# Kernel tuning notes

Hardware: AMD Instinct MI355X
Metric: run time of the kernel (lower is better)

Reference implementation:

```python
import jax, jax.numpy as jnp
import numpy as np

B, S, C = 16, 1024, 1024
E, H = 1024, 16
DH = E // H

def setup_inputs() -> dict:
    key = jax.random.key(0)
    k1, k2, k3, k4, k5 = jax.random.split(key, 5)
    x = jax.random.normal(k1, (B, S, C), dtype=jnp.float32)
    # learned params, sized per init_kwargs (torch Linear default init scale ~ 1/sqrt(fan_in))
    w_qkv = jax.random.normal(k2, (C, 3 * E), dtype=jnp.float32) / np.sqrt(C)
    b_qkv = jax.random.normal(k3, (3 * E,), dtype=jnp.float32) * 0.01
    w_o = jax.random.normal(k4, (E, E), dtype=jnp.float32) / np.sqrt(E)
    b_o = jax.random.normal(k5, (E,), dtype=jnp.float32) * 0.01
    return {"x": x, "w_qkv": w_qkv, "b_qkv": b_qkv, "w_o": w_o, "b_o": b_o}

def reference(x, w_qkv, b_qkv, w_o, b_o):
    b, s, _ = x.shape
    # fused QKV projection: [B,S,3E] -> [B,S,H,3*Dh]
    qkv = (jnp.einsum('bsc,ce->bse', x, w_qkv) + b_qkv).reshape(b, s, H, 3 * DH)
    q, k, v = jnp.split(qkv, 3, axis=-1)  # each [B,S,H,Dh]
    # NOTE: faithful to source — attention over the HEADS axis at each position,
    # scaled by embed_size**-0.5 (not head_dim).
    attn = jnp.einsum('bshd,bstd->bsht', q, k) * (E ** -0.5)  # [B,S,H,H]
    attn = jax.nn.softmax(attn, axis=-1)
    out = jnp.einsum('bsht,bstd->bshd', attn, v).reshape(b, s, E)
    return jnp.einsum('bse,ef->bsf', out, w_o) + b_o
```

## Files before the change

kernel.cpp:

```cpp
#include <hip/hip_runtime.h>
#include <hip/hip_bf16.h>
#include <stdint.h>

#define DEVINLINE __device__ __forceinline__

typedef __attribute__((ext_vector_type(4))) float f32x4;
typedef __attribute__((ext_vector_type(8))) short bf16x8;

DEVINLINE unsigned short f2bf(float f) {
    union { float f; uint32_t u; } v; v.f = f;
    uint32_t u = v.u;
    uint32_t rounding = 0x7FFFu + ((u >> 16) & 1u);
    u += rounding;
    return (unsigned short)(u >> 16);
}

DEVINLINE float bf2f(unsigned short h) {
    union { uint32_t u; float f; } v; v.u = ((uint32_t)h) << 16;
    return v.f;
}

__global__ void cvt_f32_bf16(const float* __restrict__ in,
                             unsigned short* __restrict__ out, int n) {
    int i = (blockIdx.x * blockDim.x + threadIdx.x) * 4;
    int stride = gridDim.x * blockDim.x * 4;
    for (; i < n; i += stride) {
        float4 v = *reinterpret_cast<const float4*>(in + i);
        ushort4 o;
        o.x = f2bf(v.x); o.y = f2bf(v.y); o.z = f2bf(v.z); o.w = f2bf(v.w);
        *reinterpret_cast<ushort4*>(out + i) = o;
    }
}

__global__ void transpose_cvt(const float* __restrict__ in,
                              unsigned short* __restrict__ out,
                              int R, int Ccols) {
    __shared__ float tile[32][33];
    int c0 = blockIdx.x * 32, r0 = blockIdx.y * 32;
    int tx = threadIdx.x, ty = threadIdx.y;
    #pragma unroll
    for (int j = 0; j < 32; j += 8)
        tile[ty + j][tx] = in[(size_t)(r0 + ty + j) * Ccols + c0 + tx];
    __syncthreads();
    #pragma unroll
    for (int j = 0; j < 32; j += 8)
        out[(size_t)(c0 + ty + j) * R + r0 + tx] = f2bf(tile[tx][ty + j]);
}


#define GLD(srcp, dstp) __builtin_amdgcn_global_load_lds( \
    (const __attribute__((address_space(1))) void*)(srcp), \
    (__attribute__((address_space(3))) void*)(dstp), 16, 0, 0)

#define STAGE(P, regionUS, srcBase, row0, kkE) do { \
    const unsigned short* _s = (srcBase) + (size_t)(row0) * K + (kkE); \
    unsigned short* _d = lds + (P) * 32768 + (regionUS) + wid * 512; \
    GLD(_s, _d); GLD(_s + (size_t)64 * K, _d + 4096); } while (0)

#define RD_A(dst, AS0, AS1, h) do { _Pragma("unroll") \
    for (int _i = 0; _i < 4; ++_i) { \
        dst[_i][0] = *(const bf16x8*)((AS0) + ((h) * 8192 + _i * 2048)); \
        dst[_i][1] = *(const bf16x8*)((AS1) + ((h) * 8192 + _i * 2048)); } } while (0)

#define RD_B(dst, BS0, BS1, nh) do { _Pragma("unroll") \
    for (int _j = 0; _j < 2; ++_j) { \
        dst[_j][0] = *(const bf16x8*)((BS0) + ((nh) * 4096 + _j * 2048)); \
        dst[_j][1] = *(const bf16x8*)((BS1) + ((nh) * 4096 + _j * 2048)); } } while (0)

#define MMA(aX, bY, mh, nh) do { \
    __builtin_amdgcn_s_setprio(1); \
    _Pragma("unroll") for (int _i = 0; _i < 4; ++_i) { \
    _Pragma("unroll") for (int _j = 0; _j < 2; ++_j) { \
        acc[(mh)*4+_i][(nh)*2+_j] = __builtin_amdgcn_mfma_f32_16x16x32_bf16( \
            aX[_i][0], bY[_j][0], acc[(mh)*4+_i][(nh)*2+_j], 0, 0, 0); \
        acc[(mh)*4+_i][(nh)*2+_j] = __builtin_amdgcn_mfma_f32_16x16x32_bf16( \
            aX[_i][1], bY[_j][1], acc[(mh)*4+_i][(nh)*2+_j], 0, 0, 0); } } \
    __builtin_amdgcn_s_setprio(0); } while (0)

#define VM4 asm volatile("s_waitcnt vmcnt(4)" ::: "memory")
#define BAR() asm volatile("s_barrier" ::: "memory")

#define KTILE(AS0c, AS1c, BS0c, BS1c, AS0n, AS1n, BS0n, BS1n, Pc, kk) do { \
    MMA(aA, bA, 0, 0); \
    RD_B(bB, BS0c, BS1c, 1); \
    BAR(); \
    MMA(aA, bB, 0, 1); \
    RD_A(aB, AS0c, AS1c, 1); \
    VM4; BAR(); \
    MMA(aB, bA, 1, 0); \
    RD_B(bA, BS0n, BS1n, 0); \
    STAGE(Pc, 16384, bSrc, 0,   kk); \
    STAGE(Pc, 24576, bSrc, 128, kk); \
    VM4; BAR(); \
    MMA(aB, bB, 1, 1); \
    RD_A(aA, AS0n, AS1n, 0); \
    STAGE(Pc, 0,     aSrc, 0,   kk); \
    STAGE(Pc, 8192,  aSrc, 128, kk); \
    BAR(); } while (0)

template <bool OUT_BF16>
__launch_bounds__(512, 2)
__global__ void gemm256(const unsigned short* __restrict__ A,
                        const unsigned short* __restrict__ Bt,
                        const float* __restrict__ bias,
                        void* __restrict__ Cout,
                        int M, int N, int K, int NTN) {
    __shared__ unsigned short lds[65536];
    const int NT = K >> 6;

    int t = threadIdx.x;
    int wid = t >> 6, lane = t & 63;
    int wr = wid >> 2, wc = wid & 3;
    int fr = lane & 15, fq = lane >> 4;

    int nwg = gridDim.x, bid = blockIdx.x;
    int cpx = nwg >> 3;
    int swz = (bid & 7) * cpx + (bid >> 3);
    int tm = swz / NTN, tn = swz % NTN;
    int bm = tm * 256, bn = tn * 256;

    int rowl = t >> 3, col8 = t & 7;
    int swzcol = (col8 ^ (rowl & 7)) << 3;
    const unsigned short* aSrc = A + (size_t)(bm + rowl) * K + swzcol;
    const unsigned short* bSrc = Bt + (size_t)(bn + rowl) * K + swzcol;

    int swzm = (fr & 7) << 3;
    int colS0 = (fq << 3) ^ swzm;
    int colS1 = (32 | (fq << 3)) ^ swzm;

    char* ldsb = (char*)lds;
    char* A00 = ldsb + ((wr * 128 + fr) << 7) + 2 * colS0;
    char* A10 = ldsb + ((wr * 128 + fr) << 7) + 2 * colS1;
    char* B00 = ldsb + ((256 + wc * 64 + fr) << 7) + 2 * colS0;
    char* B10 = ldsb + ((256 + wc * 64 + fr) << 7) + 2 * colS1;
    char* A01 = A00 + 65536; char* A11 = A10 + 65536;
    char* B01 = B00 + 65536; char* B11 = B10 + 65536;

    f32x4 acc[8][4] = {};
    bf16x8 aA[4][2], aB[4][2], bA[2][2], bB[2][2];

    STAGE(0, 0,     aSrc, 0,   0);
    STAGE(0, 8192,  aSrc, 128, 0);
    STAGE(0, 16384, bSrc, 0,   0);
    STAGE(0, 24576, bSrc, 128, 0);
    STAGE(1, 16384, bSrc, 0,   64);
    STAGE(1, 24576, bSrc, 128, 64);
    STAGE(1, 0,     aSrc, 0,   64);
    STAGE(1, 8192,  aSrc, 128, 64);
    asm volatile("s_waitcnt vmcnt(8)" ::: "memory");
    BAR();
    RD_A(aA, A00, A10, 0);
    RD_B(bA, B00, B10, 0);

    for (int tau = 0; tau < NT; tau += 2) {
        int kkA = ((tau + 2 < NT) ? (tau + 2) : (NT - 1)) << 6;
        KTILE(A00, A10, B00, B10, A01, A11, B01, B11, 0, kkA);
        int kkB = ((tau + 3 < NT) ? (tau + 3) : (NT - 1)) << 6;
        KTILE(A01, A11, B01, B11, A00, A10, B00, B10, 1, kkB);
    }
    asm volatile("s_waitcnt vmcnt(0)" ::: "memory");

    #pragma unroll
    for (int m = 0; m < 8; ++m) {
        #pragma unroll
        for (int n = 0; n < 4; ++n) {
            int col = bn + wc * 64 + n * 16 + fr;
            float bv = bias[col];
            #pragma unroll
            for (int r = 0; r < 4; ++r) {
                int row = bm + wr * 128 + m * 16 + fq * 4 + r;
                float v = acc[m][n][r] + bv;
                if (OUT_BF16)
                    ((unsigned short*)Cout)[(size_t)row * N + col] = f2bf(v);
                else
                    ((float*)Cout)[(size_t)row * N + col] = v;
            }
        }
    }
}

__global__ __launch_bounds__(256)
void attn_kernel(const unsigned short* __restrict__ qkv,
                 unsigned short* __restrict__ out) {
    __shared__ float sv[4][16][68];
    __shared__ float sp[4][16][17];
    int wv = threadIdx.x >> 6;
    int l = threadIdx.x & 63;
    int pos = blockIdx.x * 4 + wv;
    const unsigned short* rowp = qkv + (size_t)pos * 3072;

    #pragma unroll
    for (int j = 0; j < 2; ++j) {
        int i8 = (j * 64 + l) * 8;
        int h = i8 >> 6, d = i8 & 63;
        ushort4 v0 = *reinterpret_cast<const ushort4*>(rowp + h * 192 + 128 + d);
        ushort4 v1 = *reinterpret_cast<const ushort4*>(rowp + h * 192 + 128 + d + 4);
        sv[wv][h][d + 0] = bf2f(v0.x); sv[wv][h][d + 1] = bf2f(v0.y);
        sv[wv][h][d + 2] = bf2f(v0.z); sv[wv][h][d + 3] = bf2f(v0.w);
        sv[wv][h][d + 4] = bf2f(v1.x); sv[wv][h][d + 5] = bf2f(v1.y);
        sv[wv][h][d + 6] = bf2f(v1.z); sv[wv][h][d + 7] = bf2f(v1.w);
    }

    int fr = l & 15, fq = l >> 4;
    const unsigned short* hb = rowp + fr * 192 + fq * 8;
    bf16x8 kf0 = *reinterpret_cast<const bf16x8*>(hb + 64);
    bf16x8 kf1 = *reinterpret_cast<const bf16x8*>(hb + 96);
    bf16x8 qf0 = *reinterpret_cast<const bf16x8*>(hb);
    bf16x8 qf1 = *reinterpret_cast<const bf16x8*>(hb + 32);
    f32x4 st = {};
    st = __builtin_amdgcn_mfma_f32_16x16x32_bf16(kf0, qf0, st, 0, 0, 0);
    st = __builtin_amdgcn_mfma_f32_16x16x32_bf16(kf1, qf1, st, 0, 0, 0);

    float s0 = st[0] * 0.03125f, s1 = st[1] * 0.03125f;
    float s2 = st[2] * 0.03125f, s3 = st[3] * 0.03125f;
    float m = fmaxf(fmaxf(s0, s1), fmaxf(s2, s3));
    m = fmaxf(m, __shfl_xor(m, 16));
    m = fmaxf(m, __shfl_xor(m, 32));
    float e0 = __expf(s0 - m), e1 = __expf(s1 - m);
    float e2 = __expf(s2 - m), e3 = __expf(s3 - m);
    float sum = e0 + e1 + e2 + e3;
    sum += __shfl_xor(sum, 16);
    sum += __shfl_xor(sum, 32);
    float inv = 1.0f / sum;
    sp[wv][fr][fq * 4 + 0] = e0 * inv;
    sp[wv][fr][fq * 4 + 1] = e1 * inv;
    sp[wv][fr][fq * 4 + 2] = e2 * inv;
    sp[wv][fr][fq * 4 + 3] = e3 * inv;
    __syncthreads();

    int h2 = l >> 2, tq = l & 3;
    int dbase = tq * 16;
    float4 o0 = {}, o1 = {}, o2 = {}, o3 = {};
    #pragma unroll
    for (int tt = 0; tt < 16; ++tt) {
        float p = sp[wv][h2][tt];
        float4 v0 = *reinterpret_cast<const float4*>(&sv[wv][tt][dbase + 0]);
        float4 v1 = *reinterpret_cast<const float4*>(&sv[wv][tt][dbase + 4]);
        float4 v2 = *reinterpret_cast<const float4*>(&sv[wv][tt][dbase + 8]);
        float4 v3 = *reinterpret_cast<const float4*>(&sv[wv][tt][dbase + 12]);
        o0.x += p * v0.x; o0.y += p * v0.y; o0.z += p * v0.z; o0.w += p * v0.w;
        o1.x += p * v1.x; o1.y += p * v1.y; o1.z += p * v1.z; o1.w += p * v1.w;
        o2.x += p * v2.x; o2.y += p * v2.y; o2.z += p * v2.z; o2.w += p * v2.w;
        o3.x += p * v3.x; o3.y += p * v3.y; o3.z += p * v3.z; o3.w += p * v3.w;
    }
    ushort4* po = (ushort4*)(out + (size_t)pos * 1024 + h2 * 64 + dbase);
    ushort4 w0 = { f2bf(o0.x), f2bf(o0.y), f2bf(o0.z), f2bf(o0.w) };
    ushort4 w1 = { f2bf(o1.x), f2bf(o1.y), f2bf(o1.z), f2bf(o1.w) };
    ushort4 w2 = { f2bf(o2.x), f2bf(o2.y), f2bf(o2.z), f2bf(o2.w) };
    ushort4 w3 = { f2bf(o3.x), f2bf(o3.y), f2bf(o3.z), f2bf(o3.w) };
    po[0] = w0; po[1] = w1; po[2] = w2; po[3] = w3;
}

extern "C" void kernel_launch(void* const* d_in, const int* in_sizes, int n_in,
                              void* d_out, int out_size, void* d_ws, size_t ws_size,
                              hipStream_t stream) {
    const float* x     = (const float*)d_in[0];
    const float* w_qkv = (const float*)d_in[1];
    const float* b_qkv = (const float*)d_in[2];
    const float* w_o   = (const float*)d_in[3];
    const float* b_o   = (const float*)d_in[4];
    float* out = (float*)d_out;

    const int C = 1024, E = 1024;
    const int M = 16 * 1024;
    const int N1 = 3 * E;

    char* ws = (char*)d_ws;
    unsigned short* xb    = (unsigned short*)ws;
    unsigned short* wqkvT = xb    + (size_t)M * C;
    unsigned short* qkv   = wqkvT + (size_t)N1 * C;
    unsigned short* woT   = qkv   + (size_t)M * N1;
    unsigned short* aout  = woT   + (size_t)E * E;

    cvt_f32_bf16<<<2048, 256, 0, stream>>>(x, xb, M * C);
    dim3 tb(32, 8);
    transpose_cvt<<<dim3(N1 / 32, C / 32), tb, 0, stream>>>(w_qkv, wqkvT, C, N1);
    transpose_cvt<<<dim3(E / 32, E / 32), tb, 0, stream>>>(w_o, woT, E, E);

    gemm256<true><<<dim3((M / 256) * (N1 / 256)), 512, 0, stream>>>(
        xb, wqkvT, b_qkv, qkv, M, N1, C, N1 / 256);
    attn_kernel<<<M / 4, 256, 0, stream>>>(qkv, aout);
    gemm256<false><<<dim3((M / 256) * (E / 256)), 512, 0, stream>>>(
        aout, woT, b_o, out, M, E, E, E / 256);
}
```

Measured before the change: 187.1 us.

## Restructure GEMM main loop into eight-phase interleaved LDS read, load, MFMA schedule

Remaps each warp's output sub-tile so that warps cover interleaved 64-row and 32-column slices of each 128-row and 128-column half. The K loop is rewritten as eight phases, each issuing one LDS fragment read plus one global-to-LDS stage, then a barrier, an lgkmcnt wait and an MFMA block. The aim is to spread memory traffic evenly across the MFMA work and release LDS buffer halves sooner, reusing B fragments in a ping-pong order. It adds many more barriers and waits per iteration, which may serialize the waves and reduce overlap.

```diff
diff --git a/kernel.cpp b/kernel.cpp
--- a/kernel.cpp
+++ b/kernel.cpp
@@ -59,13 +59,13 @@
 
 #define RD_A(dst, AS0, AS1, h) do { _Pragma("unroll") \
     for (int _i = 0; _i < 4; ++_i) { \
-        dst[_i][0] = *(const bf16x8*)((AS0) + ((h) * 8192 + _i * 2048)); \
-        dst[_i][1] = *(const bf16x8*)((AS1) + ((h) * 8192 + _i * 2048)); } } while (0)
+        dst[_i][0] = *(const bf16x8*)((AS0) + ((h) * 16384 + _i * 2048)); \
+        dst[_i][1] = *(const bf16x8*)((AS1) + ((h) * 16384 + _i * 2048)); } } while (0)
 
 #define RD_B(dst, BS0, BS1, nh) do { _Pragma("unroll") \
     for (int _j = 0; _j < 2; ++_j) { \
-        dst[_j][0] = *(const bf16x8*)((BS0) + ((nh) * 4096 + _j * 2048)); \
-        dst[_j][1] = *(const bf16x8*)((BS1) + ((nh) * 4096 + _j * 2048)); } } while (0)
+        dst[_j][0] = *(const bf16x8*)((BS0) + ((nh) * 16384 + _j * 2048)); \
+        dst[_j][1] = *(const bf16x8*)((BS1) + ((nh) * 16384 + _j * 2048)); } } while (0)
 
 #define MMA(aX, bY, mh, nh) do { \
     __builtin_amdgcn_s_setprio(1); \
@@ -77,26 +77,9 @@
             aX[_i][1], bY[_j][1], acc[(mh)*4+_i][(nh)*2+_j], 0, 0, 0); } } \
     __builtin_amdgcn_s_setprio(0); } while (0)
 
-#define VM4 asm volatile("s_waitcnt vmcnt(4)" ::: "memory")
+#define VM6 asm volatile("s_waitcnt vmcnt(6)" ::: "memory")
+#define LG0 asm volatile("s_waitcnt lgkmcnt(0)" ::: "memory")
 #define BAR() asm volatile("s_barrier" ::: "memory")
-
-#define KTILE(AS0c, AS1c, BS0c, BS1c, AS0n, AS1n, BS0n, BS1n, Pc, kk) do { \
-    MMA(aA, bA, 0, 0); \
-    RD_B(bB, BS0c, BS1c, 1); \
-    BAR(); \
-    MMA(aA, bB, 0, 1); \
-    RD_A(aB, AS0c, AS1c, 1); \
-    VM4; BAR(); \
-    MMA(aB, bA, 1, 0); \
-    RD_B(bA, BS0n, BS1n, 0); \
-    STAGE(Pc, 16384, bSrc, 0,   kk); \
-    STAGE(Pc, 24576, bSrc, 128, kk); \
-    VM4; BAR(); \
-    MMA(aB, bB, 1, 1); \
-    RD_A(aA, AS0n, AS1n, 0); \
-    STAGE(Pc, 0,     aSrc, 0,   kk); \
-    STAGE(Pc, 8192,  aSrc, 128, kk); \
-    BAR(); } while (0)
 
 template <bool OUT_BF16>
 __launch_bounds__(512, 2)
@@ -129,46 +112,63 @@
     int colS1 = (32 | (fq << 3)) ^ swzm;
 
     char* ldsb = (char*)lds;
-    char* A00 = ldsb + ((wr * 128 + fr) << 7) + 2 * colS0;
-    char* A10 = ldsb + ((wr * 128 + fr) << 7) + 2 * colS1;
-    char* B00 = ldsb + ((256 + wc * 64 + fr) << 7) + 2 * colS0;
-    char* B10 = ldsb + ((256 + wc * 64 + fr) << 7) + 2 * colS1;
+    char* A00 = ldsb + ((wr * 64 + fr) << 7) + 2 * colS0;
+    char* A10 = ldsb + ((wr * 64 + fr) << 7) + 2 * colS1;
+    char* B00 = ldsb + 32768 + ((wc * 32 + fr) << 7) + 2 * colS0;
+    char* B10 = ldsb + 32768 + ((wc * 32 + fr) << 7) + 2 * colS1;
     char* A01 = A00 + 65536; char* A11 = A10 + 65536;
     char* B01 = B00 + 65536; char* B11 = B10 + 65536;
 
     f32x4 acc[8][4] = {};
     bf16x8 aA[4][2], aB[4][2], bA[2][2], bB[2][2];
 
+    STAGE(0, 16384, bSrc, 0,   0);
     STAGE(0, 0,     aSrc, 0,   0);
+    STAGE(0, 24576, bSrc, 128, 0);
     STAGE(0, 8192,  aSrc, 128, 0);
-    STAGE(0, 16384, bSrc, 0,   0);
-    STAGE(0, 24576, bSrc, 128, 0);
     STAGE(1, 16384, bSrc, 0,   64);
+    STAGE(1, 0,     aSrc, 0,   64);
     STAGE(1, 24576, bSrc, 128, 64);
-    STAGE(1, 0,     aSrc, 0,   64);
     STAGE(1, 8192,  aSrc, 128, 64);
-    asm volatile("s_waitcnt vmcnt(8)" ::: "memory");
+    VM6;
     BAR();
-    RD_A(aA, A00, A10, 0);
-    RD_B(bA, B00, B10, 0);
+    RD_B(bB, B00, B10, 0);
+    LG0;
+    BAR();
 
     for (int tau = 0; tau < NT; tau += 2) {
-        int kkA = ((tau + 2 < NT) ? (tau + 2) : (NT - 1)) << 6;
-        KTILE(A00, A10, B00, B10, A01, A11, B01, B11, 0, kkA);
-        int kkB = ((tau + 3 < NT) ? (tau + 3) : (NT - 1)) << 6;
-        KTILE(A01, A11, B01, B11, A00, A10, B00, B10, 1, kkB);
+        int kkE = ((tau + 2 < NT) ? (tau + 2) : (NT - 1)) << 6;
+        int kkO = ((tau + 3 < NT) ? (tau + 3) : (NT - 1)) << 6;
+        RD_A(aA, A00, A10, 0);  STAGE(0, 16384, bSrc, 0,   kkE);
+        BAR(); LG0; MMA(aA, bB, 0, 0); BAR();
+        RD_B(bA, B00, B10, 1);  STAGE(0, 0,     aSrc, 0,   kkE);
+        BAR(); LG0; MMA(aA, bA, 0, 1); BAR();
+        RD_A(aB, A00, A10, 1);  STAGE(0, 24576, bSrc, 128, kkE);
+        BAR(); LG0; MMA(aB, bA, 1, 1); BAR();
+        RD_B(bA, B01, B11, 0);  STAGE(0, 8192,  aSrc, 128, kkE);
+        BAR(); LG0; MMA(aB, bB, 1, 0); VM6; BAR();
+        RD_A(aA, A01, A11, 0);  STAGE(1, 16384, bSrc, 0,   kkO);
+        BAR(); LG0; MMA(aA, bA, 0, 0); BAR();
+        RD_B(bB, B01, B11, 1);  STAGE(1, 0,     aSrc, 0,   kkO);
+        BAR(); LG0; MMA(aA, bB, 0, 1); BAR();
+        RD_A(aB, A01, A11, 1);  STAGE(1, 24576, bSrc, 128, kkO);
+        BAR(); LG0; MMA(aB, bB, 1, 1); BAR();
+        RD_B(bB, B00, B10, 0);  STAGE(1, 8192,  aSrc, 128, kkO);
+        BAR(); LG0; MMA(aB, bA, 1, 0); VM6; BAR();
     }
     asm volatile("s_waitcnt vmcnt(0)" ::: "memory");
 
     #pragma unroll
     for (int m = 0; m < 8; ++m) {
+        int h = m >> 2, i = m & 3;
         #pragma unroll
         for (int n = 0; n < 4; ++n) {
-            int col = bn + wc * 64 + n * 16 + fr;
+            int nh = n >> 1, j = n & 1;
+            int col = bn + nh * 128 + wc * 32 + j * 16 + fr;
             float bv = bias[col];
             #pragma unroll
             for (int r = 0; r < 4; ++r) {
-                int row = bm + wr * 128 + m * 16 + fq * 4 + r;
+                int row = bm + h * 128 + wr * 64 + i * 16 + fq * 4 + r;
                 float v = acc[m][n][r] + bv;
                 if (OUT_BF16)
                     ((unsigned short*)Cout)[(size_t)row * N + col] = f2bf(v);
```

After: 193.9 us. +3.7%, slower.
